# Kernel optimization log

Measured on AMD Instinct MI355X. Metric: run time of the kernel, lower is better.

The kernel has to match this reference:

```python
import jax, jax.numpy as jnp
import numpy as np

B, T, D, H, E, M = 4, 2048, 2048, 8, 512, 8  # batch, seq, hidden, moe_heads, moe_experts, moe_dim//2
F = E * M  # flatten_shape = 4096
HALF = D // 2


def act(z):
    # 'relu2' activation: relu(x)**2
    r = jax.nn.relu(z)
    return r * r


def setup_inputs() -> dict:
    key = jax.random.key(0)
    ks = jax.random.split(key, 13)
    s = 0.02
    return {
        "x": jax.random.normal(ks[0], (B, T, D), jnp.float32),
        "g1": jax.random.uniform(ks[1], (B, T, H, E), jnp.float32),
        "g2": jax.random.uniform(ks[2], (B, T, H, E), jnp.float32),
        "u1_w": jax.random.normal(ks[3], (F, D), jnp.float32) * s,
        "u1_b": jnp.zeros((F,), jnp.float32),
        "u2_w": jax.random.normal(ks[4], (F, D), jnp.float32) * s,
        "u2_b": jnp.zeros((F,), jnp.float32),
        "v11_w": jax.random.normal(ks[5], (HALF, F), jnp.float32) * s,
        "v12_w": jax.random.normal(ks[6], (HALF, F), jnp.float32) * s,
        "v21_w": jax.random.normal(ks[7], (HALF, F), jnp.float32) * s,
        "v22_w": jax.random.normal(ks[8], (HALF, F), jnp.float32) * s,
        "b1": jax.random.normal(ks[9], (E, HALF), jnp.float32) * s,
        "b2": jax.random.normal(ks[10], (E, HALF), jnp.float32) * s,
    }


def reference(x, g1, g2, u1_w, u1_b, u2_w, u2_b, v11_w, v12_w, v21_w, v22_w, b1, b2):
    # x1, x2: [B,T,E,M]
    x1 = act(x @ u1_w.T + u1_b).reshape(B, T, E, M)
    x2 = act(x @ u2_w.T + u2_b).reshape(B, T, E, M)

    g1s = g1.sum(axis=2)  # [B,T,E] (einsum '...hi->...i')
    g2s = g2.sum(axis=2)

    # x11 = v11(einsum('btim,bthi->btim', x1, g1).flatten(-2))
    x11 = (x1 * g1s[..., None]).reshape(B, T, F) @ v11_w.T
    # x12 = v12(einsum('btjm,bthj,bthi->btim', x2, g2, g1).flatten(-2))
    t2 = jnp.einsum('btjm,bthj->bthm', x2, g2)
    x12 = jnp.einsum('bthm,bthi->btim', t2, g1).reshape(B, T, F) @ v12_w.T
    # x13 = einsum('bthi,id->btd', g1, b1)
    x13 = g1s @ b1

    # x21 = v21(einsum('btim,bthi,bthj->btjm', x1, g1, g2).flatten(-2))
    t1 = jnp.einsum('btim,bthi->bthm', x1, g1)
    x21 = jnp.einsum('bthm,bthj->btjm', t1, g2).reshape(B, T, F) @ v21_w.T
    # x22 = v22(einsum('btjm,bthj->btjm', x2, g2).flatten(-2))
    x22 = (x2 * g2s[..., None]).reshape(B, T, F) @ v22_w.T
    # x23 = einsum('bthj,jd->btd', g2, b2)
    x23 = g2s @ b2

    return jnp.concatenate((x11 + x12 + x13, x21 + x22 + x23), axis=-1)
```

## Files before the change

### kernel.cpp

```cpp
#include <hip/hip_runtime.h>
#include <hip/hip_bf16.h>

#define TOK   8192
#define DD    2048
#define FF    4096
#define EE    512
#define HALF  1024
#define KCAT  8704

typedef __bf16 bf16x8 __attribute__((ext_vector_type(8)));
typedef __bf16 bf16x4 __attribute__((ext_vector_type(4)));
typedef float  f32x4  __attribute__((ext_vector_type(4)));
using bf16 = __hip_bfloat16;

#define AS1(p) ((const __attribute__((address_space(1))) void*)(p))
#define AS3(p) ((__attribute__((address_space(3))) void*)(p))

#define PR0 4194304u
#define PR1 6291456u
#define PR2 8388608u
__global__ __launch_bounds__(256)
void prep_cvt(const float* __restrict__ x, const float* __restrict__ u1_w,
              const float* __restrict__ u2_w,
              bf16* __restrict__ Xb, bf16* __restrict__ U1b, bf16* __restrict__ U2b)
{
    const unsigned stride = gridDim.x * blockDim.x;
    for (unsigned i = blockIdx.x * blockDim.x + threadIdx.x; i < PR2; i += stride) {
        const float* src; bf16* dst; unsigned s;
        if (i < PR0)      { s = i;        src = x;    dst = Xb;  }
        else if (i < PR1) { s = i - PR0;  src = u1_w; dst = U1b; }
        else              { s = i - PR1;  src = u2_w; dst = U2b; }
        float4 v = ((const float4*)src)[s];
        bf16x4 o;
        o[0] = (__bf16)v.x; o[1] = (__bf16)v.y; o[2] = (__bf16)v.z; o[3] = (__bf16)v.w;
        ((bf16x4*)dst)[s] = o;
    }
}

template<int MODE>
__global__ __launch_bounds__(512, 2)
void gemmP(const bf16* __restrict__ A0, const bf16* __restrict__ B0,
           const float* __restrict__ bias0, void* __restrict__ C0,
           const bf16* __restrict__ A1, const bf16* __restrict__ B1,
           const float* __restrict__ bias1, void* __restrict__ C1,
           int nbm, int nbn, int K, int ldc,
           const float* __restrict__ xv11, const float* __restrict__ xv12,
           const float* __restrict__ xv21, const float* __restrict__ xv22,
           const float* __restrict__ xb1, const float* __restrict__ xb2,
           bf16* __restrict__ xWl, bf16* __restrict__ xWr)
{
    __shared__ __align__(16) char smem[131072];
    const int tid  = threadIdx.x;
    const int npg  = nbm * nbn;

    if (MODE == 1 && blockIdx.x >= (unsigned)(2 * npg)) {
        const unsigned lane_g = (blockIdx.x - 2 * npg) * 512u + tid;
        #pragma unroll 4
        for (int k = 0; k < 32; ++k) {
            unsigned w = lane_g + (unsigned)k * 131072u;
            const bool left = w < 2097152u;
            unsigned s = left ? w : w - 2097152u;
            unsigned n = s >> 11, j = s & 2047u;
            const float* vs = left ? (j < 1024u ? xv11 : xv12) : (j < 1024u ? xv21 : xv22);
            unsigned jj = (j < 1024u) ? j : (j - 1024u);
            float4 v = *(const float4*)(vs + (size_t)n * FF + jj * 4);
            bf16x4 o;
            o[0] = (__bf16)v.x; o[1] = (__bf16)v.y; o[2] = (__bf16)v.z; o[3] = (__bf16)v.w;
            bf16* wb = left ? xWl : xWr;
            *(bf16x4*)(wb + (size_t)n * KCAT + ((j < 1024u) ? 0 : FF) + jj * 4) = o;
        }
        #pragma unroll 2
        for (int k = 0; k < 8; ++k) {
            unsigned w = lane_g + (unsigned)k * 131072u;
            const bool left = w < 524288u;
            unsigned r = left ? w : w - 524288u;
            unsigned n = r >> 9, e = r & 511u;
            const float* bm = left ? xb1 : xb2;
            bf16* wb = left ? xWl : xWr;
            wb[(size_t)n * KCAT + 2 * FF + e] = __float2bfloat16(bm[(size_t)e * HALF + n]);
        }
        return;
    }

    const int lane = tid & 63;
    const int wid  = tid >> 6;
    const int wm = wid >> 2, wn = wid & 3;
    const int r16 = lane & 15, kb = lane >> 4;

    int bid = blockIdx.x;
    {
        int nwg = 2 * npg;
        int q = nwg >> 3, r = nwg & 7;
        int xcd = bid & 7, idx = bid >> 3;
        bid = (xcd < r ? xcd * (q + 1) : r * (q + 1) + (xcd - r) * q) + idx;
    }
    const int g   = bid / npg;
    const int lb  = bid - g * npg;
    const int bm = lb / nbn, bn = lb - bm * nbn;

    const bf16*  A    = g ? A1 : A0;
    const bf16*  Bw   = g ? B1 : B0;
    const float* bias = g ? bias1 : bias0;
    char* Cout = (char*)(g ? C1 : C0);

    const long row0 = (long)bm * 256;
    const int  col0 = bn * 256;
    const int  nt   = K >> 6;

    const char* gA[2]; const char* gB[2];
    #pragma unroll
    for (int l = 0; l < 2; ++l) {
        const uint32_t S = (uint32_t)(l * 512 + tid) * 16;
        const int r  = (int)(S >> 6);
        const int cb = (int)((S & 63) ^ ((uint32_t)((r >> 1) & 3) << 4));
        gA[l] = (const char*)A  + (row0 + r) * (long)K * 2 + cb;
        gB[l] = (const char*)Bw + (long)(col0 + r) * K * 2 + cb;
    }
    const uint32_t ldst = (uint32_t)(tid & ~63) * 16;

    const uint32_t swz  = ((uint32_t)(r16 >> 1) & 3u) << 4;
    const uint32_t aoff = (uint32_t)((wm * 128 + r16) * 64 + kb * 16) ^ swz;
    const uint32_t boff = (uint32_t)((wn * 64  + r16) * 64 + kb * 16) ^ swz;

    f32x4 acc[8][4];
    #pragma unroll
    for (int i = 0; i < 8; ++i)
        #pragma unroll
        for (int j = 0; j < 4; ++j)
            acc[i][j] = (f32x4){0.f, 0.f, 0.f, 0.f};

    __builtin_amdgcn_global_load_lds(AS1(gA[0]),      AS3(smem +     0 + ldst), 16, 0, 0);
    __builtin_amdgcn_global_load_lds(AS1(gA[1]),      AS3(smem +  8192 + ldst), 16, 0, 0);
    __builtin_amdgcn_global_load_lds(AS1(gB[0]),      AS3(smem + 32768 + ldst), 16, 0, 0);
    __builtin_amdgcn_global_load_lds(AS1(gB[1]),      AS3(smem + 40960 + ldst), 16, 0, 0);
    __builtin_amdgcn_global_load_lds(AS1(gA[0] + 64), AS3(smem + 16384 + ldst), 16, 0, 0);
    __builtin_amdgcn_global_load_lds(AS1(gA[1] + 64), AS3(smem + 24576 + ldst), 16, 0, 0);
    __builtin_amdgcn_global_load_lds(AS1(gB[0] + 64), AS3(smem + 49152 + ldst), 16, 0, 0);
    __builtin_amdgcn_global_load_lds(AS1(gB[1] + 64), AS3(smem + 57344 + ldst), 16, 0, 0);
    asm volatile("s_waitcnt vmcnt(4)" ::: "memory");
    __builtin_amdgcn_s_barrier();

    bf16x8 afA[4], afB[4], bv0[4], bv1[4];
    #pragma unroll
    for (int f = 0; f < 4; ++f) {
        afA[f] = *(const bf16x8*)(smem +     0 + aoff + f * 1024);
        bv0[f] = *(const bf16x8*)(smem + 32768 + boff + f * 1024);
    }

#define MFMA16(AF, BV, IH)                                                              \
    _Pragma("unroll")                                                                   \
    for (int fi = 0; fi < 4; ++fi) {                                                    \
        acc[(IH)*4+fi][0] = __builtin_amdgcn_mfma_f32_16x16x32_bf16(AF[fi], BV[0], acc[(IH)*4+fi][0], 0, 0, 0); \
        acc[(IH)*4+fi][1] = __builtin_amdgcn_mfma_f32_16x16x32_bf16(AF[fi], BV[1], acc[(IH)*4+fi][1], 0, 0, 0); \
        acc[(IH)*4+fi][2] = __builtin_amdgcn_mfma_f32_16x16x32_bf16(AF[fi], BV[2], acc[(IH)*4+fi][2], 0, 0, 0); \
        acc[(IH)*4+fi][3] = __builtin_amdgcn_mfma_f32_16x16x32_bf16(AF[fi], BV[3], acc[(IH)*4+fi][3], 0, 0, 0); \
    }

    for (int t = 0; t < nt; ++t) {
        const char* pb = smem + (t & 1) * 65536;
        char*       pt = smem + ((t + 1) & 1) * 65536;
        const bool  st = (t + 1 < nt);
        const long  koff = (long)(t + 1) * 128;

        if (st) {
            __builtin_amdgcn_global_load_lds(AS1(gA[0] + koff), AS3(pt +    0 + ldst), 16, 0, 0);
            __builtin_amdgcn_global_load_lds(AS1(gA[1] + koff), AS3(pt + 8192 + ldst), 16, 0, 0);
        }
        __builtin_amdgcn_s_barrier();
        #pragma unroll
        for (int f = 0; f < 4; ++f)
            afB[f] = *(const bf16x8*)(pb + 4096 + aoff + f * 1024);
        MFMA16(afA, bv0, 0)

        if (st) {
            __builtin_amdgcn_global_load_lds(AS1(gB[0] + koff), AS3(pt + 32768 + ldst), 16, 0, 0);
            __builtin_amdgcn_global_load_lds(AS1(gB[1] + koff), AS3(pt + 40960 + ldst), 16, 0, 0);
            asm volatile("s_waitcnt vmcnt(4)" ::: "memory");
        } else {
            asm volatile("s_waitcnt vmcnt(0)" ::: "memory");
        }
        __builtin_amdgcn_s_barrier();
        #pragma unroll
        for (int f = 0; f < 4; ++f) {
            afA[f] = *(const bf16x8*)(pb + 16384 + aoff + f * 1024);
            bv1[f] = *(const bf16x8*)(pb + 49152 + boff + f * 1024);
        }
        MFMA16(afB, bv0, 1)

        if (st) {
            __builtin_amdgcn_global_load_lds(AS1(gA[0] + koff + 64), AS3(pt + 16384 + ldst), 16, 0, 0);
            __builtin_amdgcn_global_load_lds(AS1(gA[1] + koff + 64), AS3(pt + 24576 + ldst), 16, 0, 0);
        }
        __builtin_amdgcn_s_barrier();
        #pragma unroll
        for (int f = 0; f < 4; ++f)
            afB[f] = *(const bf16x8*)(pb + 16384 + 4096 + aoff + f * 1024);
        MFMA16(afA, bv1, 0)

        if (st) {
            __builtin_amdgcn_global_load_lds(AS1(gB[0] + koff + 64), AS3(pt + 49152 + ldst), 16, 0, 0);
            __builtin_amdgcn_global_load_lds(AS1(gB[1] + koff + 64), AS3(pt + 57344 + ldst), 16, 0, 0);
            asm volatile("s_waitcnt vmcnt(4)" ::: "memory");
        }
        __builtin_amdgcn_s_barrier();
        if (st) {
            #pragma unroll
            for (int f = 0; f < 4; ++f) {
                afA[f] = *(const bf16x8*)(pt +     0 + aoff + f * 1024);
                bv0[f] = *(const bf16x8*)(pt + 32768 + boff + f * 1024);
            }
        }
        MFMA16(afB, bv1, 1)
    }
#undef MFMA16

    const int rb = (lane >> 4) * 4;
    #pragma unroll
    for (int i = 0; i < 8; ++i) {
        #pragma unroll
        for (int j = 0; j < 4; ++j) {
            const int cc = col0 + wn * 64 + j * 16 + r16;
            float badd = 0.f;
            if (MODE == 1) badd = bias[cc];
            #pragma unroll
            for (int e = 0; e < 4; ++e) {
                long row = row0 + wm * 128 + i * 16 + rb + e;
                float v = acc[i][j][e];
                if (MODE == 1) {
                    v += badd;
                    v = fmaxf(v, 0.f);
                    v = v * v;
                    ((bf16*)Cout)[row * ldc + cc] = __float2bfloat16(v);
                } else {
                    ((float*)Cout)[row * ldc + cc] = v;
                }
            }
        }
    }
}

#define GPAD 524
__global__ __launch_bounds__(256)
void glue(const float* __restrict__ g1, const float* __restrict__ g2,
          bf16* __restrict__ Yl, bf16* __restrict__ Yr)
{
    __shared__ __align__(16) float g1t[8 * GPAD];
    __shared__ __align__(16) float g2t[8 * GPAD];
    __shared__ float g1s[EE], g2s[EE];
    __shared__ float t1s[64], t2s[64];
    __shared__ float t1p[4][64], t2p[4][64];
    __shared__ __align__(16) bf16 x1t[FF], x2t[FF];

    const int t   = blockIdx.x;
    const int tid = threadIdx.x;
    const float* g1p = g1 + (size_t)t * FF;
    const float* g2p = g2 + (size_t)t * FF;
    bf16* ylp = Yl + (size_t)t * KCAT;
    bf16* yrp = Yr + (size_t)t * KCAT;

    #pragma unroll
    for (int c = 0; c < 4; ++c) {
        int idx4 = (c * 256 + tid) * 4;
        float4 v1 = *(const float4*)(g1p + idx4);
        float4 v2 = *(const float4*)(g2p + idx4);
        int h = idx4 >> 9, e = idx4 & 511;
        *(float4*)&g1t[h * GPAD + e] = v1;
        *(float4*)&g2t[h * GPAD + e] = v2;
    }
    #pragma unroll
    for (int c = 0; c < 2; ++c) {
        int idx8 = (c * 256 + tid) * 8;
        *(bf16x8*)&x1t[idx8] = *(const bf16x8*)(ylp + idx8);
        *(bf16x8*)&x2t[idx8] = *(const bf16x8*)(yrp + FF + idx8);
    }
    __syncthreads();

    #pragma unroll
    for (int c = 0; c < 2; ++c) {
        int e = c * 256 + tid;
        float s1 = 0.f, s2 = 0.f;
        #pragma unroll
        for (int h = 0; h < 8; ++h) { s1 += g1t[h * GPAD + e]; s2 += g2t[h * GPAD + e]; }
        g1s[e] = s1; g2s[e] = s2;
    }

    {
        int o = tid & 63;
        int h = o & 7, m = o >> 3;
        int p = tid >> 6;
        float s1 = 0.f, s2 = 0.f;
        #pragma unroll 8
        for (int ii = 0; ii < 128; ++ii) {
            int e = p * 128 + ii;
            float xv1 = __bfloat162float(x1t[e * 8 + m]);
            float xv2 = __bfloat162float(x2t[e * 8 + m]);
            s1 += xv1 * g1t[h * GPAD + e];
            s2 += xv2 * g2t[h * GPAD + e];
        }
        t1p[p][o] = s1; t2p[p][o] = s2;
    }
    __syncthreads();
    if (tid < 64)       t1s[tid] = t1p[0][tid] + t1p[1][tid] + t1p[2][tid] + t1p[3][tid];
    else if (tid < 128) { int o = tid - 64; t2s[o] = t2p[0][o] + t2p[1][o] + t2p[2][o] + t2p[3][o]; }
    __syncthreads();

    #pragma unroll
    for (int c = 0; c < 2; ++c) {
        int f0 = (c * 256 + tid) * 8;
        int e  = f0 >> 3;
        float s1 = g1s[e], s2 = g2s[e];
        bf16x8 xa = *(const bf16x8*)&x1t[f0];
        bf16x8 xb = *(const bf16x8*)&x2t[f0];
        bf16x8 o1, o2;
        #pragma unroll
        for (int u = 0; u < 8; ++u) {
            o1[u] = (__bf16)((float)xa[u] * s1);
            o2[u] = (__bf16)((float)xb[u] * s2);
        }
        *(bf16x8*)(ylp + f0)      = o1;
        *(bf16x8*)(yrp + FF + f0) = o2;
    }
    #pragma unroll
    for (int c = 0; c < 2; ++c) {
        int f0 = (c * 256 + tid) * 8;
        int i  = f0 >> 3;
        bf16x8 o12v, o21v;
        #pragma unroll
        for (int m = 0; m < 8; ++m) {
            float s12 = 0.f, s21 = 0.f;
            #pragma unroll
            for (int h = 0; h < 8; ++h) {
                s12 += t2s[(m << 3) | h] * g1t[h * GPAD + i];
                s21 += t1s[(m << 3) | h] * g2t[h * GPAD + i];
            }
            o12v[m] = (__bf16)s12;
            o21v[m] = (__bf16)s21;
        }
        *(bf16x8*)(ylp + FF + f0) = o12v;
        *(bf16x8*)(yrp + f0)      = o21v;
    }
    {
        int e0 = tid * 2;
        ylp[2 * FF + e0]     = __float2bfloat16(g1s[e0]);
        ylp[2 * FF + e0 + 1] = __float2bfloat16(g1s[e0 + 1]);
        yrp[2 * FF + e0]     = __float2bfloat16(g2s[e0]);
        yrp[2 * FF + e0 + 1] = __float2bfloat16(g2s[e0 + 1]);
    }
}


extern "C" void kernel_launch(void* const* d_in, const int* in_sizes, int n_in,
                              void* d_out, int out_size, void* d_ws, size_t ws_size,
                              hipStream_t stream) {
    const float* x    = (const float*)d_in[0];
    const float* g1   = (const float*)d_in[1];
    const float* g2   = (const float*)d_in[2];
    const float* u1_w = (const float*)d_in[3];
    const float* u1_b = (const float*)d_in[4];
    const float* u2_w = (const float*)d_in[5];
    const float* u2_b = (const float*)d_in[6];
    const float* v11  = (const float*)d_in[7];
    const float* v12  = (const float*)d_in[8];
    const float* v21  = (const float*)d_in[9];
    const float* v22  = (const float*)d_in[10];
    const float* b1   = (const float*)d_in[11];
    const float* b2   = (const float*)d_in[12];
    float* out = (float*)d_out;

    size_t off = 0;
    char* base = (char*)d_ws;
    auto take = [&](size_t bytes) { void* p = base + off; off += (bytes + 255) & ~(size_t)255; return p; };
    bf16* Xb  = (bf16*)take((size_t)TOK * DD * 2);
    bf16* U1b = (bf16*)take((size_t)FF * DD * 2);
    bf16* U2b = (bf16*)take((size_t)FF * DD * 2);
    bf16* Wl  = (bf16*)take((size_t)HALF * KCAT * 2);
    bf16* Wr  = (bf16*)take((size_t)HALF * KCAT * 2);
    bf16* Yl  = (bf16*)take((size_t)TOK * KCAT * 2);
    bf16* Yr  = (bf16*)take((size_t)TOK * KCAT * 2);

    prep_cvt<<<2048, 256, 0, stream>>>(x, u1_w, u2_w, Xb, U1b, U2b);

    gemmP<1><<<2 * (TOK / 256) * (FF / 256) + 256, 512, 0, stream>>>(
        Xb, U1b, u1_b, Yl,
        Xb, U2b, u2_b, Yr + FF,
        TOK / 256, FF / 256, DD, KCAT,
        v11, v12, v21, v22, b1, b2, Wl, Wr);

    glue<<<TOK, 256, 0, stream>>>(g1, g2, Yl, Yr);

    gemmP<0><<<2 * (TOK / 256) * (HALF / 256), 512, 0, stream>>>(
        Yl, Wl, nullptr, out,
        Yr, Wr, nullptr, out + HALF,
        TOK / 256, HALF / 256, KCAT, DD,
        nullptr, nullptr, nullptr, nullptr, nullptr, nullptr, nullptr, nullptr);
}
```

Before: 677.2 us.

## Restructure GEMM mainloop into 4-stage K=32 LDS ring with deeper prefetch

The GEMM mainloop previously double-buffered 64-wide K tiles across two 64KB LDS halves. It now uses 32-wide K steps with a four-slot 32KB ring and issues global-to-LDS loads three tiles ahead, with vmcnt waits graded by how many tiles remain. The goal is to hide more global-memory latency behind MFMA work. The cost is a barrier every half-tile, and the unroll-by-two loop assumes nt is even.

```diff
diff --git a/kernel.cpp b/kernel.cpp
--- a/kernel.cpp
+++ b/kernel.cpp
@@ -39,7 +39,7 @@
 
 template<int MODE>
 __global__ __launch_bounds__(512, 2)
-void gemmP(const bf16* __restrict__ A0, const bf16* __restrict__ B0,
+void gemmD(const bf16* __restrict__ A0, const bf16* __restrict__ B0,
            const float* __restrict__ bias0, void* __restrict__ C0,
            const bf16* __restrict__ A1, const bf16* __restrict__ B1,
            const float* __restrict__ bias1, void* __restrict__ C1,
@@ -105,7 +105,7 @@
 
     const long row0 = (long)bm * 256;
     const int  col0 = bn * 256;
-    const int  nt   = K >> 6;
+    const int  nt   = K >> 5;
 
     const char* gA[2]; const char* gB[2];
     #pragma unroll
@@ -129,90 +129,78 @@
         for (int j = 0; j < 4; ++j)
             acc[i][j] = (f32x4){0.f, 0.f, 0.f, 0.f};
 
-    __builtin_amdgcn_global_load_lds(AS1(gA[0]),      AS3(smem +     0 + ldst), 16, 0, 0);
-    __builtin_amdgcn_global_load_lds(AS1(gA[1]),      AS3(smem +  8192 + ldst), 16, 0, 0);
-    __builtin_amdgcn_global_load_lds(AS1(gB[0]),      AS3(smem + 32768 + ldst), 16, 0, 0);
-    __builtin_amdgcn_global_load_lds(AS1(gB[1]),      AS3(smem + 40960 + ldst), 16, 0, 0);
-    __builtin_amdgcn_global_load_lds(AS1(gA[0] + 64), AS3(smem + 16384 + ldst), 16, 0, 0);
-    __builtin_amdgcn_global_load_lds(AS1(gA[1] + 64), AS3(smem + 24576 + ldst), 16, 0, 0);
-    __builtin_amdgcn_global_load_lds(AS1(gB[0] + 64), AS3(smem + 49152 + ldst), 16, 0, 0);
-    __builtin_amdgcn_global_load_lds(AS1(gB[1] + 64), AS3(smem + 57344 + ldst), 16, 0, 0);
-    asm volatile("s_waitcnt vmcnt(4)" ::: "memory");
-    __builtin_amdgcn_s_barrier();
-
-    bf16x8 afA[4], afB[4], bv0[4], bv1[4];
-    #pragma unroll
-    for (int f = 0; f < 4; ++f) {
-        afA[f] = *(const bf16x8*)(smem +     0 + aoff + f * 1024);
-        bv0[f] = *(const bf16x8*)(smem + 32768 + boff + f * 1024);
-    }
-
-#define MFMA16(AF, BV, IH)                                                              \
-    _Pragma("unroll")                                                                   \
-    for (int fi = 0; fi < 4; ++fi) {                                                    \
+#define ST_A(BUF, KO)                                                                     \
+    __builtin_amdgcn_global_load_lds(AS1(gA[0] + (KO)), AS3(smem + (BUF) +     0 + ldst), 16, 0, 0); \
+    __builtin_amdgcn_global_load_lds(AS1(gA[1] + (KO)), AS3(smem + (BUF) +  8192 + ldst), 16, 0, 0);
+#define ST_B(BUF, KO)                                                                     \
+    __builtin_amdgcn_global_load_lds(AS1(gB[0] + (KO)), AS3(smem + (BUF) + 16384 + ldst), 16, 0, 0); \
+    __builtin_amdgcn_global_load_lds(AS1(gB[1] + (KO)), AS3(smem + (BUF) + 24576 + ldst), 16, 0, 0);
+
+#define MFMA16(AF, BV, IH)                                                                \
+    _Pragma("unroll")                                                                     \
+    for (int fi = 0; fi < 4; ++fi) {                                                      \
         acc[(IH)*4+fi][0] = __builtin_amdgcn_mfma_f32_16x16x32_bf16(AF[fi], BV[0], acc[(IH)*4+fi][0], 0, 0, 0); \
         acc[(IH)*4+fi][1] = __builtin_amdgcn_mfma_f32_16x16x32_bf16(AF[fi], BV[1], acc[(IH)*4+fi][1], 0, 0, 0); \
         acc[(IH)*4+fi][2] = __builtin_amdgcn_mfma_f32_16x16x32_bf16(AF[fi], BV[2], acc[(IH)*4+fi][2], 0, 0, 0); \
         acc[(IH)*4+fi][3] = __builtin_amdgcn_mfma_f32_16x16x32_bf16(AF[fi], BV[3], acc[(IH)*4+fi][3], 0, 0, 0); \
     }
 
-    for (int t = 0; t < nt; ++t) {
-        const char* pb = smem + (t & 1) * 65536;
-        char*       pt = smem + ((t + 1) & 1) * 65536;
-        const bool  st = (t + 1 < nt);
-        const long  koff = (long)(t + 1) * 128;
-
-        if (st) {
-            __builtin_amdgcn_global_load_lds(AS1(gA[0] + koff), AS3(pt +    0 + ldst), 16, 0, 0);
-            __builtin_amdgcn_global_load_lds(AS1(gA[1] + koff), AS3(pt + 8192 + ldst), 16, 0, 0);
-        }
-        __builtin_amdgcn_s_barrier();
-        #pragma unroll
-        for (int f = 0; f < 4; ++f)
-            afB[f] = *(const bf16x8*)(pb + 4096 + aoff + f * 1024);
-        MFMA16(afA, bv0, 0)
-
-        if (st) {
-            __builtin_amdgcn_global_load_lds(AS1(gB[0] + koff), AS3(pt + 32768 + ldst), 16, 0, 0);
-            __builtin_amdgcn_global_load_lds(AS1(gB[1] + koff), AS3(pt + 40960 + ldst), 16, 0, 0);
-            asm volatile("s_waitcnt vmcnt(4)" ::: "memory");
-        } else {
-            asm volatile("s_waitcnt vmcnt(0)" ::: "memory");
-        }
-        __builtin_amdgcn_s_barrier();
-        #pragma unroll
-        for (int f = 0; f < 4; ++f) {
-            afA[f] = *(const bf16x8*)(pb + 16384 + aoff + f * 1024);
-            bv1[f] = *(const bf16x8*)(pb + 49152 + boff + f * 1024);
-        }
-        MFMA16(afB, bv0, 1)
-
-        if (st) {
-            __builtin_amdgcn_global_load_lds(AS1(gA[0] + koff + 64), AS3(pt + 16384 + ldst), 16, 0, 0);
-            __builtin_amdgcn_global_load_lds(AS1(gA[1] + koff + 64), AS3(pt + 24576 + ldst), 16, 0, 0);
-        }
-        __builtin_amdgcn_s_barrier();
-        #pragma unroll
-        for (int f = 0; f < 4; ++f)
-            afB[f] = *(const bf16x8*)(pb + 16384 + 4096 + aoff + f * 1024);
-        MFMA16(afA, bv1, 0)
-
-        if (st) {
-            __builtin_amdgcn_global_load_lds(AS1(gB[0] + koff + 64), AS3(pt + 49152 + ldst), 16, 0, 0);
-            __builtin_amdgcn_global_load_lds(AS1(gB[1] + koff + 64), AS3(pt + 57344 + ldst), 16, 0, 0);
-            asm volatile("s_waitcnt vmcnt(4)" ::: "memory");
-        }
-        __builtin_amdgcn_s_barrier();
-        if (st) {
-            #pragma unroll
-            for (int f = 0; f < 4; ++f) {
-                afA[f] = *(const bf16x8*)(pt +     0 + aoff + f * 1024);
-                bv0[f] = *(const bf16x8*)(pt + 32768 + boff + f * 1024);
-            }
-        }
-        MFMA16(afB, bv1, 1)
-    }
+    bf16x8 afLo[4], afHi[4], bvE[4], bvO[4];
+
+    ST_A(0u, 0) ST_B(0u, 0)
+    ST_A(32768u, 64)  ST_B(32768u, 64)
+    ST_A(65536u, 128) ST_B(65536u, 128)
+    asm volatile("s_waitcnt vmcnt(8)" ::: "memory");
+    __builtin_amdgcn_s_barrier();
+    #pragma unroll
+    for (int f = 0; f < 4; ++f) {
+        afLo[f] = *(const bf16x8*)(smem + aoff + f * 1024);
+        bvE[f]  = *(const bf16x8*)(smem + 16384 + boff + f * 1024);
+    }
+
+#define TILE(T, BVC, BVN)                                                                 \
+    {                                                                                     \
+        const int t_ = (T);                                                               \
+        const uint32_t bufc = ((uint32_t)(t_ & 3)) << 15;                                 \
+        const uint32_t bufn = ((uint32_t)((t_ + 1) & 3)) << 15;                           \
+        const uint32_t bufp = ((uint32_t)((t_ + 3) & 3)) << 15;                           \
+        const long kp = (long)(t_ + 3) * 64;                                              \
+        const bool sp = (t_ + 3 < nt);                                                    \
+                                \
+        if (sp) { ST_A(bufp, kp) }                                                        \
+        __builtin_amdgcn_s_barrier();                                                     \
+        _Pragma("unroll")                                                                 \
+        for (int f = 0; f < 4; ++f)                                                       \
+            afHi[f] = *(const bf16x8*)(smem + bufc + aoff + (4 + f) * 1024);              \
+        MFMA16(afLo, BVC, 0)                                                              \
+             \
+        if (sp) {                                                                         \
+            ST_B(bufp, kp)                                                                \
+            asm volatile("s_waitcnt vmcnt(8)" ::: "memory");         \
+        } else if (t_ + 2 < nt) {                                                         \
+            asm volatile("s_waitcnt vmcnt(4)" ::: "memory");                              \
+        } else if (t_ + 1 < nt) {                                                         \
+            asm volatile("s_waitcnt vmcnt(0)" ::: "memory");                              \
+        }                                                                                 \
+        __builtin_amdgcn_s_barrier();                                                     \
+        if (t_ + 1 < nt) {                                                                \
+            _Pragma("unroll")                                                             \
+            for (int f = 0; f < 4; ++f) {                                                 \
+                afLo[f] = *(const bf16x8*)(smem + bufn + aoff + f * 1024);                \
+                BVN[f]  = *(const bf16x8*)(smem + bufn + 16384 + boff + f * 1024);        \
+            }                                                                             \
+        }                                                                                 \
+        MFMA16(afHi, BVC, 1)                                                              \
+    }
+
+    for (int t = 0; t < nt; t += 2) {
+        TILE(t,     bvE, bvO)
+        TILE(t + 1, bvO, bvE)
+    }
+#undef TILE
 #undef MFMA16
+#undef ST_A
+#undef ST_B
 
     const int rb = (lane >> 4) * 4;
     #pragma unroll
@@ -380,7 +368,7 @@
 
     prep_cvt<<<2048, 256, 0, stream>>>(x, u1_w, u2_w, Xb, U1b, U2b);
 
-    gemmP<1><<<2 * (TOK / 256) * (FF / 256) + 256, 512, 0, stream>>>(
+    gemmD<1><<<2 * (TOK / 256) * (FF / 256) + 256, 512, 0, stream>>>(
         Xb, U1b, u1_b, Yl,
         Xb, U2b, u2_b, Yr + FF,
         TOK / 256, FF / 256, DD, KCAT,
@@ -388,7 +376,7 @@
 
     glue<<<TOK, 256, 0, stream>>>(g1, g2, Yl, Yr);
 
-    gemmP<0><<<2 * (TOK / 256) * (HALF / 256), 512, 0, stream>>>(
+    gemmD<0><<<2 * (TOK / 256) * (HALF / 256), 512, 0, stream>>>(
         Yl, Wl, nullptr, out,
         Yr, Wr, nullptr, out + HALF,
         TOK / 256, HALF / 256, KCAT, DD,
```

Result: no change. 680.5 us (+0.5%).
